# Performance work log

Hardware: AMD Instinct MI355X
Metric: run time of the kernel (lower is better)

Reference implementation:

```python
import jax, jax.numpy as jnp
import numpy as np


def setup_inputs() -> dict:
    key = jax.random.key(0)
    k1, k2, k3 = jax.random.split(key, 3)
    batch, h, num_logical, n_pairs = 2048, 128, 64, 512
    # P: (batch, h, h) soft assignment (approximately doubly stochastic via row softmax)
    P = jax.nn.softmax(jax.random.uniform(k1, (batch, h, h), dtype=jnp.float32) * 4.0, axis=-1)
    # d_error: (h, h) precomputed nonnegative error-distance matrix, symmetric w/ zero diag
    d = jax.random.uniform(k2, (h, h), dtype=jnp.float32)
    d_error = (d + d.T) * (1.0 - jnp.eye(h, dtype=jnp.float32))
    circuit_edge_pairs = jax.random.randint(k3, (n_pairs, 2), 0, num_logical, dtype=jnp.int64)
    return {"P": P, "d_error": d_error, "circuit_edge_pairs": circuit_edge_pairs, "num_logical": num_logical}


def reference(P, d_error, circuit_edge_pairs, num_logical):
    # Restrict to logical-qubit rows, then gather both endpoints of every circuit edge.
    P_logical = P[:, :num_logical, :]                      # (b, L, h)
    P_i = P_logical[:, circuit_edge_pairs[:, 0], :]        # (b, E, h)
    P_j = P_logical[:, circuit_edge_pairs[:, 1], :]        # (b, E, h)
    # cost[b,e] = sum_{p,q} P_i[b,e,p] * d_error[p,q] * P_j[b,e,q]
    cost = jnp.einsum('bep,pq,beq->be', P_i, d_error, P_j)
    # sum_e mean_b(cost) / E == mean over (b, e)
    return jnp.mean(cost)
```

## Files before the change

kernel.cpp:

```cpp
#include <hip/hip_runtime.h>
#include <hip/hip_bf16.h>

#define B_TOTAL 2048
#define H 128
#define NL 64
#define NPAIRS 512
#define BPB 2
#define NBLOCKS (B_TOTAL / BPB)

typedef __attribute__((ext_vector_type(8))) short bf16x8;
typedef __attribute__((ext_vector_type(4))) float f32x4;

static __device__ __forceinline__ ushort f2bf(float f) {
    uint u = __float_as_uint(f);
    u += 0x7fffu + ((u >> 16) & 1u);
    return (ushort)(u >> 16);
}
static __device__ __forceinline__ uint pk2bf(float x, float y) {
    return (uint)f2bf(x) | ((uint)f2bf(y) << 16);
}

__global__ void prep_kernel(const int* __restrict__ pairs,
                            const float* __restrict__ Dsrc,
                            float* __restrict__ Sf,
                            ushort* __restrict__ Dbf) {
    const int tid = threadIdx.x;
    if (blockIdx.x == 0) {
        __shared__ int cnt[NL * NL];
        for (int k = tid; k < NL * NL; k += 256) cnt[k] = 0;
        __syncthreads();
        for (int e = tid; e < NPAIRS; e += 256) {
            int i = pairs[2 * e] & (NL - 1);
            int j = pairs[2 * e + 1] & (NL - 1);
            atomicAdd(&cnt[i * NL + j], 1);
        }
        __syncthreads();
        for (int k = tid; k < NL * NL; k += 256) Sf[k] = (float)cnt[k];
    } else {
        int k = (blockIdx.x - 1) * 256 + tid;
        Dbf[k] = f2bf(Dsrc[k]);
    }
}

__global__ __launch_bounds__(256, 2)
void edge_loss_v3(const float* __restrict__ P,
                  const float* __restrict__ Sf,
                  const ushort* __restrict__ Dbf,
                  float* __restrict__ out) {
    __shared__ ushort lds[40960];
    ushort* Db  = lds;
    ushort* Ab0 = lds + 16384;
    ushort* Ab1 = lds + 16384 + 8192;
    ushort* Ub  = lds + 16384 + 16384;

    const int tid  = threadIdx.x;
    const int lane = tid & 63;
    const int w    = tid >> 6;
    const int l15  = lane & 15;
    const int lg   = lane >> 4;
    const uint rmask = (uint)(l15 & 7) << 4;
    const int rowa = 16 * w + l15;

    {
        const uint4* src = reinterpret_cast<const uint4*>(Dbf);
        for (int k = tid; k < 2048; k += 256) {
            int row = k >> 4, gc = k & 15;
            int gs = gc ^ (row & 7);
            *reinterpret_cast<uint4*>((char*)Db + row * 256 + gs * 16) = src[k];
        }
    }

    float sreg[4][4];
#pragma unroll
    for (int nt = 0; nt < 4; ++nt)
#pragma unroll
        for (int r = 0; r < 4; ++r)
            sreg[nt][r] = Sf[(16 * w + 4 * lg + r) * NL + nt * 16 + l15];

    f32x4 m[4];
#pragma unroll
    for (int nt = 0; nt < 4; ++nt) m[nt] = (f32x4)0.0f;

    float4 pf[8];
    const int b0 = blockIdx.x * BPB;
    auto loadA = [&](int b) {
        const float4* src = reinterpret_cast<const float4*>(P + (size_t)b * H * H);
#pragma unroll
        for (int k = 0; k < 8; ++k) pf[k] = src[tid + k * 256];
    };
    auto cvtStore = [&](ushort* dst) {
#pragma unroll
        for (int k = 0; k < 8; ++k) {
            int f4 = tid + k * 256;
            int i  = f4 >> 5;
            int q4 = (f4 & 31) * 4;
            uint2 d2;
            d2.x = pk2bf(pf[k].x, pf[k].y);
            d2.y = pk2bf(pf[k].z, pf[k].w);
            *reinterpret_cast<uint2*>((char*)dst + i * 256 + ((q4 * 2) ^ ((i & 7) << 4))) = d2;
        }
    };

    loadA(b0);
    cvtStore(Ab0);
    __syncthreads();

    for (int bb = 0; bb < BPB; ++bb) {
        const ushort* A_ = (bb & 1) ? Ab1 : Ab0;
        if (bb + 1 < BPB) loadA(b0 + bb + 1);

        f32x4 u[8];
#pragma unroll
        for (int nt = 0; nt < 8; ++nt) u[nt] = (f32x4)0.0f;
#pragma unroll
        for (int ks = 0; ks < 4; ++ks) {
            const uint koff = (uint)(ks * 64 + lg * 16);
            bf16x8 a = *reinterpret_cast<const bf16x8*>((const char*)A_ + rowa * 256 + (koff ^ rmask));
#pragma unroll
            for (int nt = 0; nt < 8; ++nt) {
                bf16x8 d = *reinterpret_cast<const bf16x8*>((const char*)Db + (nt * 16 + l15) * 256 + (koff ^ rmask));
                u[nt] = __builtin_amdgcn_mfma_f32_16x16x32_bf16(a, d, u[nt], 0, 0, 0);
            }
        }
#pragma unroll
        for (int nt = 0; nt < 8; ++nt)
#pragma unroll
            for (int r = 0; r < 4; ++r) {
                int row = 16 * w + 4 * lg + r;
                *reinterpret_cast<ushort*>((char*)Ub + row * 256 +
                    (((uint)((nt * 16 + l15) * 2)) ^ ((uint)(row & 7) << 4))) = f2bf(u[nt][r]);
            }
#pragma unroll
        for (int ks = 0; ks < 4; ++ks) {
            const uint koff = (uint)(ks * 64 + lg * 16);
            bf16x8 a2 = *reinterpret_cast<const bf16x8*>((const char*)Ub + rowa * 256 + (koff ^ rmask));
#pragma unroll
            for (int nt = 0; nt < 4; ++nt) {
                bf16x8 bf = *reinterpret_cast<const bf16x8*>((const char*)A_ + (nt * 16 + l15) * 256 + (koff ^ rmask));
                m[nt] = __builtin_amdgcn_mfma_f32_16x16x32_bf16(a2, bf, m[nt], 0, 0, 0);
            }
        }
        if (bb + 1 < BPB) {
            cvtStore((bb & 1) ? Ab0 : Ab1);
            __syncthreads();
        }
    }

    float s = 0.0f;
#pragma unroll
    for (int nt = 0; nt < 4; ++nt)
#pragma unroll
        for (int r = 0; r < 4; ++r) s = fmaf(m[nt][r], sreg[nt][r], s);
#pragma unroll
    for (int off = 32; off > 0; off >>= 1) s += __shfl_down(s, off, 64);

    __syncthreads();
    float* wsum = reinterpret_cast<float*>(Db);
    if (lane == 0) wsum[w] = s;
    __syncthreads();
    if (tid == 0)
        atomicAdd(out, (wsum[0] + wsum[1] + wsum[2] + wsum[3]) *
                       (1.0f / ((float)B_TOTAL * (float)NPAIRS)));
}

extern "C" void kernel_launch(void* const* d_in, const int* in_sizes, int n_in,
                              void* d_out, int out_size, void* d_ws, size_t ws_size,
                              hipStream_t stream) {
    const float* P     = (const float*)d_in[0];
    const float* Dsrc  = (const float*)d_in[1];
    const int*   pairs = (const int*)d_in[2];
    float* out = (float*)d_out;

    float*  Sf  = (float*)d_ws;
    ushort* Dbf = (ushort*)((char*)d_ws + NL * NL * 4);

    hipMemsetAsync(d_out, 0, sizeof(float), stream);
    prep_kernel<<<65, 256, 0, stream>>>(pairs, Dsrc, Sf, Dbf);
    edge_loss_v3<<<NBLOCKS, 256, 0, stream>>>(P, Sf, Dbf, out);
}
```

Baseline: 192.6 us.

## Use one batch per block, keep D in registers, and replace atomics with partials reduce

Each block now handles a single batch element (2048 blocks) instead of two with double buffering. The bf16 D matrix is loaded straight into registers, so LDS shrinks from 80KB to 32KB and launch bounds ask for 3 blocks per CU. The first GEMM is also repartitioned so each wave computes a 64x32 column slice, with a 16-row swizzle. The global atomicAdd and memset are replaced by per-block partials plus a single-block finish kernel. This costs one extra launch and drops the load/compute overlap that the two-batch loop provided, relying on higher occupancy instead.

```diff
diff --git a/kernel.cpp b/kernel.cpp
--- a/kernel.cpp
+++ b/kernel.cpp
@@ -5,8 +5,6 @@
 #define H 128
 #define NL 64
 #define NPAIRS 512
-#define BPB 2
-#define NBLOCKS (B_TOTAL / BPB)
 
 typedef __attribute__((ext_vector_type(8))) short bf16x8;
 typedef __attribute__((ext_vector_type(4))) float f32x4;
@@ -42,32 +40,37 @@
     }
 }
 
-__global__ __launch_bounds__(256, 2)
-void edge_loss_v3(const float* __restrict__ P,
+__global__ __launch_bounds__(256, 3)
+void edge_loss_v4(const float* __restrict__ P,
                   const float* __restrict__ Sf,
                   const ushort* __restrict__ Dbf,
-                  float* __restrict__ out) {
-    __shared__ ushort lds[40960];
-    ushort* Db  = lds;
-    ushort* Ab0 = lds + 16384;
-    ushort* Ab1 = lds + 16384 + 8192;
-    ushort* Ub  = lds + 16384 + 16384;
+                  float* __restrict__ partials) {
+    __shared__ __align__(16) ushort Ab[NL * H];
+    __shared__ __align__(16) ushort Ub[NL * H];
+    __shared__ float wsum[4];
 
     const int tid  = threadIdx.x;
     const int lane = tid & 63;
     const int w    = tid >> 6;
     const int l15  = lane & 15;
     const int lg   = lane >> 4;
-    const uint rmask = (uint)(l15 & 7) << 4;
-    const int rowa = 16 * w + l15;
+    const uint rmask = (uint)l15 << 4;
+    const int b    = blockIdx.x;
 
+    float4 pf[8];
     {
-        const uint4* src = reinterpret_cast<const uint4*>(Dbf);
-        for (int k = tid; k < 2048; k += 256) {
-            int row = k >> 4, gc = k & 15;
-            int gs = gc ^ (row & 7);
-            *reinterpret_cast<uint4*>((char*)Db + row * 256 + gs * 16) = src[k];
-        }
+        const float4* src = reinterpret_cast<const float4*>(P + (size_t)b * H * H);
+#pragma unroll
+        for (int k = 0; k < 8; ++k) pf[k] = src[tid + k * 256];
+    }
+
+    bf16x8 dreg[2][4];
+#pragma unroll
+    for (int c2 = 0; c2 < 2; ++c2) {
+        const int drow = (2 * w + c2) * 16 + l15;
+#pragma unroll
+        for (int ks = 0; ks < 4; ++ks)
+            dreg[c2][ks] = *reinterpret_cast<const bf16x8*>(Dbf + drow * H + ks * 32 + lg * 8);
     }
 
     float sreg[4][4];
@@ -77,72 +80,54 @@
         for (int r = 0; r < 4; ++r)
             sreg[nt][r] = Sf[(16 * w + 4 * lg + r) * NL + nt * 16 + l15];
 
+#pragma unroll
+    for (int k = 0; k < 8; ++k) {
+        const int f4 = tid + k * 256;
+        const int i  = f4 >> 5;
+        const uint cb = (uint)(f4 & 31) * 8;
+        uint2 d2;
+        d2.x = pk2bf(pf[k].x, pf[k].y);
+        d2.y = pk2bf(pf[k].z, pf[k].w);
+        *reinterpret_cast<uint2*>((char*)Ab + i * 256 + (cb ^ ((uint)(i & 15) << 4))) = d2;
+    }
+    __syncthreads();
+
+    f32x4 u[4][2];
+#pragma unroll
+    for (int it = 0; it < 4; ++it) { u[it][0] = (f32x4)0.0f; u[it][1] = (f32x4)0.0f; }
+#pragma unroll
+    for (int ks = 0; ks < 4; ++ks) {
+        const uint koff = (uint)(ks * 64 + lg * 16);
+#pragma unroll
+        for (int it = 0; it < 4; ++it) {
+            bf16x8 a = *reinterpret_cast<const bf16x8*>((const char*)Ab + (it * 16 + l15) * 256 + (koff ^ rmask));
+            u[it][0] = __builtin_amdgcn_mfma_f32_16x16x32_bf16(a, dreg[0][ks], u[it][0], 0, 0, 0);
+            u[it][1] = __builtin_amdgcn_mfma_f32_16x16x32_bf16(a, dreg[1][ks], u[it][1], 0, 0, 0);
+        }
+    }
+#pragma unroll
+    for (int it = 0; it < 4; ++it)
+#pragma unroll
+        for (int c2 = 0; c2 < 2; ++c2)
+#pragma unroll
+            for (int r = 0; r < 4; ++r) {
+                const int row = it * 16 + 4 * lg + r;
+                const uint cb = (uint)((2 * w + c2) * 16 + l15) * 2;
+                *reinterpret_cast<ushort*>((char*)Ub + row * 256 + (cb ^ ((uint)(row & 15) << 4))) = f2bf(u[it][c2][r]);
+            }
+    __syncthreads();
+
     f32x4 m[4];
 #pragma unroll
     for (int nt = 0; nt < 4; ++nt) m[nt] = (f32x4)0.0f;
-
-    float4 pf[8];
-    const int b0 = blockIdx.x * BPB;
-    auto loadA = [&](int b) {
-        const float4* src = reinterpret_cast<const float4*>(P + (size_t)b * H * H);
 #pragma unroll
-        for (int k = 0; k < 8; ++k) pf[k] = src[tid + k * 256];
-    };
-    auto cvtStore = [&](ushort* dst) {
+    for (int ks = 0; ks < 4; ++ks) {
+        const uint koff = (uint)(ks * 64 + lg * 16);
+        bf16x8 a2 = *reinterpret_cast<const bf16x8*>((const char*)Ub + (16 * w + l15) * 256 + (koff ^ rmask));
 #pragma unroll
-        for (int k = 0; k < 8; ++k) {
-            int f4 = tid + k * 256;
-            int i  = f4 >> 5;
-            int q4 = (f4 & 31) * 4;
-            uint2 d2;
-            d2.x = pk2bf(pf[k].x, pf[k].y);
-            d2.y = pk2bf(pf[k].z, pf[k].w);
-            *reinterpret_cast<uint2*>((char*)dst + i * 256 + ((q4 * 2) ^ ((i & 7) << 4))) = d2;
-        }
-    };
-
-    loadA(b0);
-    cvtStore(Ab0);
-    __syncthreads();
-
-    for (int bb = 0; bb < BPB; ++bb) {
-        const ushort* A_ = (bb & 1) ? Ab1 : Ab0;
-        if (bb + 1 < BPB) loadA(b0 + bb + 1);
-
-        f32x4 u[8];
-#pragma unroll
-        for (int nt = 0; nt < 8; ++nt) u[nt] = (f32x4)0.0f;
-#pragma unroll
-        for (int ks = 0; ks < 4; ++ks) {
-            const uint koff = (uint)(ks * 64 + lg * 16);
-            bf16x8 a = *reinterpret_cast<const bf16x8*>((const char*)A_ + rowa * 256 + (koff ^ rmask));
-#pragma unroll
-            for (int nt = 0; nt < 8; ++nt) {
-                bf16x8 d = *reinterpret_cast<const bf16x8*>((const char*)Db + (nt * 16 + l15) * 256 + (koff ^ rmask));
-                u[nt] = __builtin_amdgcn_mfma_f32_16x16x32_bf16(a, d, u[nt], 0, 0, 0);
-            }
-        }
-#pragma unroll
-        for (int nt = 0; nt < 8; ++nt)
-#pragma unroll
-            for (int r = 0; r < 4; ++r) {
-                int row = 16 * w + 4 * lg + r;
-                *reinterpret_cast<ushort*>((char*)Ub + row * 256 +
-                    (((uint)((nt * 16 + l15) * 2)) ^ ((uint)(row & 7) << 4))) = f2bf(u[nt][r]);
-            }
-#pragma unroll
-        for (int ks = 0; ks < 4; ++ks) {
-            const uint koff = (uint)(ks * 64 + lg * 16);
-            bf16x8 a2 = *reinterpret_cast<const bf16x8*>((const char*)Ub + rowa * 256 + (koff ^ rmask));
-#pragma unroll
-            for (int nt = 0; nt < 4; ++nt) {
-                bf16x8 bf = *reinterpret_cast<const bf16x8*>((const char*)A_ + (nt * 16 + l15) * 256 + (koff ^ rmask));
-                m[nt] = __builtin_amdgcn_mfma_f32_16x16x32_bf16(a2, bf, m[nt], 0, 0, 0);
-            }
-        }
-        if (bb + 1 < BPB) {
-            cvtStore((bb & 1) ? Ab0 : Ab1);
-            __syncthreads();
+        for (int nt = 0; nt < 4; ++nt) {
+            bf16x8 bfr = *reinterpret_cast<const bf16x8*>((const char*)Ab + (nt * 16 + l15) * 256 + (koff ^ rmask));
+            m[nt] = __builtin_amdgcn_mfma_f32_16x16x32_bf16(a2, bfr, m[nt], 0, 0, 0);
         }
     }
 
@@ -154,13 +139,29 @@
 #pragma unroll
     for (int off = 32; off > 0; off >>= 1) s += __shfl_down(s, off, 64);
 
+    if (lane == 0) wsum[w] = s;
     __syncthreads();
-    float* wsum = reinterpret_cast<float*>(Db);
+    if (tid == 0) partials[b] = wsum[0] + wsum[1] + wsum[2] + wsum[3];
+}
+
+__global__ void finish_kernel(const float* __restrict__ partials,
+                              float* __restrict__ out) {
+    __shared__ float wsum[4];
+    const int tid = threadIdx.x, lane = tid & 63, w = tid >> 6;
+    const float4* p4 = reinterpret_cast<const float4*>(partials);
+    float s = 0.0f;
+#pragma unroll
+    for (int k = 0; k < 2; ++k) {
+        float4 v = p4[tid + k * 256];
+        s += v.x + v.y + v.z + v.w;
+    }
+#pragma unroll
+    for (int off = 32; off > 0; off >>= 1) s += __shfl_down(s, off, 64);
     if (lane == 0) wsum[w] = s;
     __syncthreads();
     if (tid == 0)
-        atomicAdd(out, (wsum[0] + wsum[1] + wsum[2] + wsum[3]) *
-                       (1.0f / ((float)B_TOTAL * (float)NPAIRS)));
+        out[0] = (wsum[0] + wsum[1] + wsum[2] + wsum[3]) *
+                 (1.0f / ((float)B_TOTAL * (float)NPAIRS));
 }
 
 extern "C" void kernel_launch(void* const* d_in, const int* in_sizes, int n_in,
@@ -171,10 +172,11 @@
     const int*   pairs = (const int*)d_in[2];
     float* out = (float*)d_out;
 
-    float*  Sf  = (float*)d_ws;
-    ushort* Dbf = (ushort*)((char*)d_ws + NL * NL * 4);
+    float*  Sf       = (float*)d_ws;
+    ushort* Dbf      = (ushort*)((char*)d_ws + NL * NL * 4);
+    float*  partials = (float*)((char*)d_ws + NL * NL * 4 + H * H * 2);
 
-    hipMemsetAsync(d_out, 0, sizeof(float), stream);
     prep_kernel<<<65, 256, 0, stream>>>(pairs, Dsrc, Sf, Dbf);
-    edge_loss_v3<<<NBLOCKS, 256, 0, stream>>>(P, Sf, Dbf, out);
+    edge_loss_v4<<<B_TOTAL, 256, 0, stream>>>(P, Sf, Dbf, partials);
+    finish_kernel<<<1, 256, 0, stream>>>(partials, out);
 }
```

Result: faster. 184.5 us (-4.2%).
